# Kernel optimization log

Measured on AMD Instinct MI355X. Metric: run time of the kernel, lower is better.

Reference implementation:

```python
import jax, jax.numpy as jnp
import numpy as np

K = 4
H = 256
N0 = 65536
SIZES = [(65536, 32768), (32768, 8192), (8192, 2048)]  # (m_l, num_segments_l)


def setup_inputs() -> dict:
    key = jax.random.key(0)
    ks = jax.random.split(key, 20)
    inp = {}
    inp["x"] = jax.random.normal(ks[0], (N0, H), jnp.float32)
    inp["initial_map"] = jax.random.randint(ks[1], (N0,), 0, N0)
    prev = N0
    for l, (m, g) in enumerate(SIZES):
        # -1 is the 'no child' sentinel (maps to the prepended zero row after +1)
        inp[f"order_matrix_{l}"] = jax.random.randint(ks[2 + l], (K, m), -1, prev)
        inp[f"pooling_{l}"] = jnp.repeat(jnp.arange(g), m // g)  # covers all segments
        inp[f"type_mask_{l}"] = jax.random.randint(ks[6 + l], (m,), 0, 4)  # 0 leaf, 1 P, 2 Z, 3 S
        prev = g
    scale = 1.0 / np.sqrt(H).astype(np.float32)
    inp["W_z"] = jax.random.normal(ks[10], (K, H, H), jnp.float32) * scale
    inp["W_z_int"] = jax.random.normal(ks[11], (H, H), jnp.float32) * scale
    inp["W_s"] = jax.random.normal(ks[12], (K, H, H), jnp.float32) * scale
    inp["W_s_int"] = jax.random.normal(ks[13], (H, H), jnp.float32) * scale
    inp["W_p"] = jax.random.normal(ks[14], (H, H), jnp.float32) * scale
    inp["W_pf"] = jax.random.normal(ks[15], (H, H), jnp.float32) * scale
    return inp


def _layer(data, om, pool, tmask, g, W_z, W_z_int, W_s, W_s_int, W_p, W_pf):
    omp = om + 1                      # [K, m]; -1 -> 0 (zero row)
    empty = omp == 0                  # children that don't exist
    padded = jnp.concatenate([jnp.zeros((1, data.shape[1]), data.dtype), data], axis=0)
    gathered = padded[omp]            # [K, m, H]

    def type_sum(W):                  # per-child Linear, mask missing children, sum over children
        stack = jnp.einsum('kmh,koh->kmo', gathered, W)
        return jnp.where(empty[:, :, None], 0.0, stack).sum(axis=0)

    z_out = type_sum(W_z) @ W_z_int.T         # [m, H]
    s_out = type_sum(W_s) @ W_s_int.T         # [m, H]
    p_out = gathered[0] @ W_p.T               # [m, H]

    temp = gathered[0]                        # default: pass through first child (leaf type 0)
    temp = jnp.where((tmask == 2)[:, None], z_out, temp)
    temp = jnp.where((tmask == 3)[:, None], s_out, temp)
    temp = jnp.where((tmask == 1)[:, None], p_out, temp)
    temp = jnp.where(empty.all(axis=0)[:, None], 0.0, temp)

    pooled = jax.ops.segment_sum(temp, pool, num_segments=g)       # global_add_pool
    tm2 = jax.ops.segment_max(tmask, pool, num_segments=g)         # global_max_pool
    pooled = jnp.where((tm2 != 0)[:, None], jax.nn.elu(pooled), pooled)
    pooled = jnp.where((tm2 == 1)[:, None], pooled @ W_pf.T, pooled)
    return pooled


def reference(x, initial_map,
              order_matrix_0, pooling_0, type_mask_0,
              order_matrix_1, pooling_1, type_mask_1,
              order_matrix_2, pooling_2, type_mask_2,
              W_z, W_z_int, W_s, W_s_int, W_p, W_pf):
    oms = [order_matrix_0, order_matrix_1, order_matrix_2]
    pools = [pooling_0, pooling_1, pooling_2]
    tmasks = [type_mask_0, type_mask_1, type_mask_2]
    data = x[initial_map]
    for l, (m, g) in enumerate(SIZES):
        data = _layer(data, oms[l], pools[l], tmasks[l], g,
                      W_z, W_z_int, W_s, W_s_int, W_p, W_pf)
    return data
```

## Files before the change

### kernel.cpp

```cpp
#include <hip/hip_runtime.h>
#include <math.h>

#define H 256

typedef __attribute__((ext_vector_type(8))) short bf16x8;
typedef __attribute__((ext_vector_type(4))) float f32x4;
typedef __attribute__((ext_vector_type(4))) short short4v;

__device__ __forceinline__ short f2bf(float f) {
  union { float f; unsigned u; } x;
  x.f = f;
  unsigned r = x.u + 0x7fffu + ((x.u >> 16) & 1u);
  return (short)(r >> 16);
}
__device__ __forceinline__ float bf2f(short s) {
  union { float f; unsigned u; } x;
  x.u = ((unsigned)(unsigned short)s) << 16;
  return x.f;
}

__global__ __launch_bounds__(256) void gather_cvt_kernel(const float4* __restrict__ x,
                                                         const int* __restrict__ map,
                                                         short4v* __restrict__ out, int n) {
  int total = n * (H / 4);
  for (int idx = blockIdx.x * blockDim.x + threadIdx.x; idx < total;
       idx += gridDim.x * blockDim.x) {
    int e = idx >> 6;
    int q = idx & 63;
    float4 v = x[(size_t)map[e] * 64 + q];
    short4v s;
    s[0] = f2bf(v.x); s[1] = f2bf(v.y); s[2] = f2bf(v.z); s[3] = f2bf(v.w);
    out[idx] = s;
  }
}

__global__ __launch_bounds__(256) void wprep_kernel(
    const float* __restrict__ Wz, const float* __restrict__ Wzint,
    const float* __restrict__ Ws, const float* __restrict__ Wsint,
    const float* __restrict__ Wp, const float* __restrict__ Wpf,
    short* __restrict__ Wbf, int* __restrict__ zero_base) {
  int bid = blockIdx.x;
  int tid = threadIdx.x;
  if (bid < 2048) {
    const float* Wint = (bid < 1024) ? Wzint : Wsint;
    const float* W1 = (bid < 1024) ? Wz : Ws;
    short* out = Wbf + ((bid < 1024) ? 131072 : 393216);
    int b = bid & 1023;
    int k = b >> 8, o = b & 255;
    const float* A = Wint + (size_t)o * 256;
    const float* B = W1 + (size_t)k * 65536;
    float acc = 0.f;
#pragma unroll 8
    for (int j = 0; j < 256; ++j) acc = fmaf(A[j], B[(size_t)j * 256 + tid], acc);
    out[((size_t)k * 256 + o) * 256 + tid] = f2bf(acc);
  } else if (bid < 2176) {
    int i4 = (bid - 2048) * 256 + tid;
    int e = i4 * 4;
    const float* src = (e < 65536) ? Wp : Wpf;
    int off = (e < 65536) ? e : e - 65536;
    float4 v = *(const float4*)(src + off);
    short4v o;
    o[0] = f2bf(v.x); o[1] = f2bf(v.y); o[2] = f2bf(v.z); o[3] = f2bf(v.w);
    *(short4v*)(Wbf + e) = o;
  } else {
    if (tid < 192) zero_base[tid] = 0;
  }
}

__device__ __forceinline__ void bucket_body(const int* __restrict__ tmask, int base,
                                            int m, int g, int r,
                                            int* __restrict__ lists,
                                            int* __restrict__ counts,
                                            int* __restrict__ tm2,
                                            int* __restrict__ listF,
                                            int* __restrict__ cntF) {
  __shared__ int lc[4];
  __shared__ int lbase[4];
  int tid = threadIdx.x;
  if (tid < 4) lc[tid] = 0;
  __syncthreads();
  int i = base * 256 + tid;
  int t = 0, rank = 0;
  bool ok = i < m;
  if (ok) {
    t = tmask[i];
    rank = atomicAdd(&lc[t], 1);
  }
  __syncthreads();
  if (tid < 4) lbase[tid] = atomicAdd(&counts[tid], lc[tid]);
  __syncthreads();
  if (ok) lists[t * m + lbase[t] + rank] = i;

  int s = i;
  if (s < g) {
    int t2 = 0;
    for (int j = 0; j < r; ++j) {
      int tt = tmask[s * r + j];
      t2 = tt > t2 ? tt : t2;
    }
    tm2[s] = t2;
    unsigned long long mask = __ballot(t2 == 1);
    if (t2 == 1) {
      int lane = tid & 63;
      unsigned long long lt = (lane == 0) ? 0ull : (~0ull >> (64 - lane));
      int rnk = __popcll(mask & lt);
      int leader = __ffsll((long long)mask) - 1;
      int b = 0;
      if (lane == leader) b = atomicAdd(cntF, __popcll(mask));
      b = __shfl(b, leader);
      listF[b + rnk] = s;
    }
  }
}

__global__ __launch_bounds__(256) void bucket_all_kernel(
    const int* __restrict__ tm0, const int* __restrict__ tm1, const int* __restrict__ tm2in,
    int* __restrict__ lists0, int* __restrict__ lists1, int* __restrict__ lists2,
    int* __restrict__ counts,
    int* __restrict__ seg0, int* __restrict__ seg1, int* __restrict__ seg2,
    int* __restrict__ listF0, int* __restrict__ listF1, int* __restrict__ listF2) {
  int bid = blockIdx.x;
  if (bid < 256)
    bucket_body(tm0, bid, 65536, 32768, 2, lists0, counts, seg0, listF0, counts + 4);
  else if (bid < 384)
    bucket_body(tm1, bid - 256, 32768, 8192, 4, lists1, counts + 8, seg1, listF1, counts + 12);
  else
    bucket_body(tm2in, bid - 384, 8192, 2048, 4, lists2, counts + 16, seg2, listF2, counts + 20);
}

template <int NCH>
__device__ __forceinline__ void gemm_tile(const short* __restrict__ Abf,
                                          const int* __restrict__ om, int m,
                                          const int* __restrict__ list, int n,
                                          int rowbase, int cg,
                                          const short* __restrict__ W1,
                                          const short* __restrict__ zrow,
                                          short* __restrict__ temp, char* lds) {
  const int tid = threadIdx.x;
  const int lane = tid & 63;
  const int wave = tid >> 6;
  const int lr = lane & 15;
  const int kg = lane >> 4;
  const int wrow = rowbase + wave * 32;

  int cidx[2][NCH];
#pragma unroll
  for (int rt = 0; rt < 2; ++rt) {
    int i = wrow + rt * 16 + lr;
    int rid = (i < n) ? list[i] : -1;
#pragma unroll
    for (int k = 0; k < NCH; ++k) cidx[rt][k] = (rid >= 0) ? om[k * m + rid] : -1;
  }

  f32x4 acc[2][4];
#pragma unroll
  for (int rt = 0; rt < 2; ++rt)
#pragma unroll
    for (int c = 0; c < 4; ++c) {
      f32x4 z = {0.f, 0.f, 0.f, 0.f};
      acc[rt][c] = z;
    }

  for (int kc = 0; kc < NCH; ++kc) {
    const short* ap[2];
#pragma unroll
    for (int rt = 0; rt < 2; ++rt) {
      int c = cidx[rt][kc];
      ap[rt] = (c >= 0) ? (Abf + (size_t)c * 256 + kg * 8) : (zrow + kg * 8);
    }

    const char* psrc = (const char*)W1 + ((size_t)kc * 256 + cg * 64) * 512;
    __syncthreads();
#pragma unroll
    for (int it = 0; it < 8; ++it) {
      int idx = it * 4096 + tid * 16;
      bf16x8 v = *(const bf16x8*)(psrc + idx);
      int col = idx >> 9;
      *(bf16x8*)(lds + (idx ^ ((col & 7) << 4))) = v;
    }
    __syncthreads();

#pragma unroll
    for (int ko = 0; ko < 8; ++ko) {
      bf16x8 a[2], b[4];
#pragma unroll
      for (int c = 0; c < 4; ++c) {
        int col = c * 16 + lr;
        int off = (col * 512 + ko * 64 + kg * 16) ^ ((col & 7) << 4);
        b[c] = *(const bf16x8*)(lds + off);
      }
#pragma unroll
      for (int rt = 0; rt < 2; ++rt) a[rt] = *(const bf16x8*)(ap[rt] + ko * 32);
#pragma unroll
      for (int rt = 0; rt < 2; ++rt)
#pragma unroll
        for (int c = 0; c < 4; ++c)
          acc[rt][c] =
              __builtin_amdgcn_mfma_f32_16x16x32_bf16(a[rt], b[c], acc[rt][c], 0, 0, 0);
    }
  }

#pragma unroll
  for (int rt = 0; rt < 2; ++rt) {
#pragma unroll
    for (int q = 0; q < 4; ++q) {
      int i2 = wrow + rt * 16 + kg * 4 + q;
      if (i2 >= n) continue;
      int row = list[i2];
      short* dst = temp + (size_t)row * 256 + cg * 64 + lr;
#pragma unroll
      for (int c = 0; c < 4; ++c) dst[c * 16] = f2bf(acc[rt][c][q]);
    }
  }
}

__global__ __launch_bounds__(256) void fused_gemm(
    const short* __restrict__ Abf, const int* __restrict__ om, int m,
    const int* __restrict__ lists, const int* __restrict__ counts,
    const short* __restrict__ Wp,
    const short* __restrict__ Wcz, const short* __restrict__ Wcs,
    const short* __restrict__ zrow,
    short* __restrict__ temp) {
  const int c14 = (m >> 7) << 2;
  int bid = (int)blockIdx.x;
  __shared__ __align__(16) char lds[64 * 512];

  int type, item;
  if (bid < c14)            { type = 2; item = bid; }
  else if (bid < 2 * c14)   { type = 3; item = bid - c14; }
  else if (bid < 3 * c14)   { type = 1; item = bid - 2 * c14; }
  else                      { type = 0; item = bid - 3 * c14; }

  int n = counts[type];
  const int* list = lists + type * m;

  if (type == 0) {
    int rowbase = item * 64;
    if (rowbase >= n) return;
    int lim = n - rowbase;
    if (lim > 64) lim = 64;
    for (int idx = threadIdx.x; idx < lim * 32; idx += 256) {
      int e = rowbase + (idx >> 5);
      int q = idx & 31;
      int row = list[e];
      int c = om[row];
      bf16x8 v = {0, 0, 0, 0, 0, 0, 0, 0};
      if (c >= 0) v = *(const bf16x8*)(Abf + (size_t)c * 256 + q * 8);
      *(bf16x8*)(temp + (size_t)row * 256 + q * 8) = v;
    }
    return;
  }

  int rowbase = (item >> 2) * 128;
  int cg = item & 3;
  if (rowbase >= n) return;

  if (type == 1)
    gemm_tile<1>(Abf, om, m, list, n, rowbase, cg, Wp, zrow, temp, lds);
  else if (type == 2)
    gemm_tile<4>(Abf, om, m, list, n, rowbase, cg, Wcz, zrow, temp, lds);
  else
    gemm_tile<4>(Abf, om, m, list, n, rowbase, cg, Wcs, zrow, temp, lds);
}

__global__ __launch_bounds__(256) void reduce_kernel(const short* __restrict__ temp,
                                                     int r, int g,
                                                     const int* __restrict__ tm2,
                                                     float* __restrict__ outf,
                                                     short* __restrict__ outbf) {
  int idx = blockIdx.x * 256 + threadIdx.x;
  if (idx >= g * 32) return;
  int s = idx >> 5;
  int q = idx & 31;
  float acc[8];
#pragma unroll
  for (int k = 0; k < 8; ++k) acc[k] = 0.f;
  for (int j = 0; j < r; ++j) {
    bf16x8 v = *(const bf16x8*)(temp + (size_t)(s * r + j) * 256 + q * 8);
#pragma unroll
    for (int k = 0; k < 8; ++k) acc[k] += bf2f(v[k]);
  }
  if (tm2[s] != 0) {
#pragma unroll
    for (int k = 0; k < 8; ++k) acc[k] = acc[k] > 0.f ? acc[k] : (expf(acc[k]) - 1.f);
  }
  if (outf) {
    float4 f0 = {acc[0], acc[1], acc[2], acc[3]};
    float4 f1 = {acc[4], acc[5], acc[6], acc[7]};
    *(float4*)(outf + (size_t)s * 256 + q * 8) = f0;
    *(float4*)(outf + (size_t)s * 256 + q * 8 + 4) = f1;
  }
  if (outbf) {
    bf16x8 o;
#pragma unroll
    for (int k = 0; k < 8; ++k) o[k] = f2bf(acc[k]);
    *(bf16x8*)(outbf + (size_t)s * 256 + q * 8) = o;
  }
}

template <int SRC>
__global__ __launch_bounds__(256) void pf_gemm(short* __restrict__ buf,
                                               float* __restrict__ fbuf,
                                               const int* __restrict__ listF,
                                               const int* __restrict__ cnt,
                                               const short* __restrict__ Wpf) {
  int n = *cnt;
  int rowbase = blockIdx.x * 32;
  if (rowbase >= n) return;
  const int lane = threadIdx.x & 63;
  const int wave = threadIdx.x >> 6;
  const int colbase = wave * 64;
  const int lr = lane & 15;
  const int kg = lane >> 4;

  int src[2];
#pragma unroll
  for (int rt = 0; rt < 2; ++rt) {
    int i = rowbase + rt * 16 + lr;
    src[rt] = (i < n) ? listF[i] : -1;
  }

  f32x4 acc[2][4];
#pragma unroll
  for (int rt = 0; rt < 2; ++rt)
#pragma unroll
    for (int c = 0; c < 4; ++c) {
      f32x4 z = {0.f, 0.f, 0.f, 0.f};
      acc[rt][c] = z;
    }

#pragma unroll 2
  for (int ko = 0; ko < 256; ko += 32) {
    bf16x8 b[4];
#pragma unroll
    for (int c = 0; c < 4; ++c)
      b[c] = *(const bf16x8*)(Wpf + (size_t)(colbase + c * 16 + lr) * 256 + ko + kg * 8);
#pragma unroll
    for (int rt = 0; rt < 2; ++rt) {
      bf16x8 a = {0, 0, 0, 0, 0, 0, 0, 0};
      if (src[rt] >= 0) {
        if (SRC == 0) {
          a = *(const bf16x8*)(buf + (size_t)src[rt] * 256 + ko + kg * 8);
        } else {
          const float* p = fbuf + (size_t)src[rt] * 256 + ko + kg * 8;
          float4 u0 = *(const float4*)p;
          float4 u1 = *(const float4*)(p + 4);
          a[0] = f2bf(u0.x); a[1] = f2bf(u0.y); a[2] = f2bf(u0.z); a[3] = f2bf(u0.w);
          a[4] = f2bf(u1.x); a[5] = f2bf(u1.y); a[6] = f2bf(u1.z); a[7] = f2bf(u1.w);
        }
      }
#pragma unroll
      for (int c = 0; c < 4; ++c)
        acc[rt][c] = __builtin_amdgcn_mfma_f32_16x16x32_bf16(a, b[c], acc[rt][c], 0, 0, 0);
    }
  }

  __syncthreads();

#pragma unroll
  for (int rt = 0; rt < 2; ++rt) {
#pragma unroll
    for (int q = 0; q < 4; ++q) {
      int i2 = rowbase + rt * 16 + kg * 4 + q;
      if (i2 >= n) continue;
      int c2 = listF[i2];
      if (SRC == 0) {
        short* db = buf + (size_t)c2 * 256 + colbase + lr;
#pragma unroll
        for (int c = 0; c < 4; ++c) db[c * 16] = f2bf(acc[rt][c][q]);
      } else {
        float* df = fbuf + (size_t)c2 * 256 + colbase + lr;
#pragma unroll
        for (int c = 0; c < 4; ++c) df[c * 16] = acc[rt][c][q];
      }
    }
  }
}

extern "C" void kernel_launch(void* const* d_in, const int* in_sizes, int n_in,
                              void* d_out, int out_size, void* d_ws, size_t ws_size,
                              hipStream_t stream) {
  const float* x = (const float*)d_in[0];
  const int* initial_map = (const int*)d_in[1];
  const int* om[3] = {(const int*)d_in[2], (const int*)d_in[5], (const int*)d_in[8]};
  const int* tmask[3] = {(const int*)d_in[4], (const int*)d_in[7], (const int*)d_in[10]};
  const float* W_z = (const float*)d_in[11];
  const float* W_z_int = (const float*)d_in[12];
  const float* W_s = (const float*)d_in[13];
  const float* W_s_int = (const float*)d_in[14];
  const float* W_p = (const float*)d_in[15];
  const float* W_pf = (const float*)d_in[16];

  char* base = (char*)d_ws;
  short* d0bf  = (short*)(base);
  short* temp0 = (short*)(base + 33554432);
  short* d1bf  = (short*)(base);
  short* temp1 = (short*)(base + 16777216);
  short* d2bf  = (short*)(base + 33554432);
  short* temp2 = (short*)(base + 37748736);
  size_t off = 67108864;
  short* Wbf = (short*)(base + off); off += 655360 * 2;
  int* lists0 = (int*)(base + off); off += 4u * 65536 * 4;
  int* lists1 = (int*)(base + off); off += 4u * 32768 * 4;
  int* lists2 = (int*)(base + off); off += 4u * 8192 * 4;
  int* listF0 = (int*)(base + off); off += 32768 * 4;
  int* listF1 = (int*)(base + off); off += 8192 * 4;
  int* listF2 = (int*)(base + off); off += 2048 * 4;
  int* seg0 = (int*)(base + off); off += 32768 * 4;
  int* seg1 = (int*)(base + off); off += 8192 * 4;
  int* seg2 = (int*)(base + off); off += 2048 * 4;
  int* counts = (int*)(base + off); off += 256;
  short* zrow = (short*)(base + off); off += 512;

  short* Wp_bf  = Wbf + 0;
  short* Wpf_bf = Wbf + 65536;
  short* Wcz_bf = Wbf + 131072;
  short* Wcs_bf = Wbf + 393216;

  hipLaunchKernelGGL(wprep_kernel, dim3(2177), dim3(256), 0, stream, W_z, W_z_int,
                     W_s, W_s_int, W_p, W_pf, Wbf, counts);
  hipLaunchKernelGGL(bucket_all_kernel, dim3(416), dim3(256), 0, stream,
                     tmask[0], tmask[1], tmask[2], lists0, lists1, lists2, counts,
                     seg0, seg1, seg2, listF0, listF1, listF2);
  hipLaunchKernelGGL(gather_cvt_kernel, dim3(2048), dim3(256), 0, stream,
                     (const float4*)x, initial_map, (short4v*)d0bf, 65536);

  const int Ms[3] = {65536, 32768, 8192};
  const int Gs[3] = {32768, 8192, 2048};
  const short* dinbf[3] = {d0bf, d1bf, d2bf};
  short* tempL[3] = {temp0, temp1, temp2};
  short* nextbf[3] = {d1bf, d2bf, nullptr};
  int* listsL[3] = {lists0, lists1, lists2};
  int* listFL[3] = {listF0, listF1, listF2};
  int* segL[3] = {seg0, seg1, seg2};

  for (int l = 0; l < 3; ++l) {
    int m = Ms[l], g = Gs[l], r = m / g;
    int c14 = (m >> 7) << 2;
    int grid = 3 * c14 + m / 64;
    hipLaunchKernelGGL(fused_gemm, dim3(grid), dim3(256), 0, stream, dinbf[l], om[l],
                       m, listsL[l], counts + l * 8, Wp_bf, Wcz_bf, Wcs_bf, zrow,
                       tempL[l]);

    hipLaunchKernelGGL(reduce_kernel, dim3(g * 32 / 256), dim3(256), 0, stream,
                       tempL[l], r, g, segL[l], (l == 2) ? (float*)d_out : nullptr,
                       nextbf[l]);

    if (l < 2)
      hipLaunchKernelGGL((pf_gemm<0>), dim3(g / 32), dim3(256), 0, stream, nextbf[l],
                         (float*)nullptr, listFL[l], counts + l * 8 + 4, Wpf_bf);
    else
      hipLaunchKernelGGL((pf_gemm<1>), dim3(g / 32), dim3(256), 0, stream,
                         (short*)nullptr, (float*)d_out, listFL[l], counts + l * 8 + 4,
                         Wpf_bf);
  }
}
```

Baseline: 229.0 us.

## Compute all 256 output columns per block to reuse gathered A rows

Each GEMM block now covers the full 256-wide output (four 64-column groups) instead of a single column group, so a block handles 128 rows at full width. The gathered child rows are loaded into registers once per child rather than being re-gathered by four separate blocks. The cost is a 4x larger accumulator array (128 floats per thread) plus 64 A registers, which raises register pressure and lowers occupancy. The grid also shrinks by 4x, leaving fewer blocks to spread across the CUs.

```diff
diff --git a/kernel.cpp b/kernel.cpp
--- a/kernel.cpp
+++ b/kernel.cpp
@@ -132,7 +132,7 @@
 __device__ __forceinline__ void gemm_tile(const short* __restrict__ Abf,
                                           const int* __restrict__ om, int m,
                                           const int* __restrict__ list, int n,
-                                          int rowbase, int cg,
+                                          int rowbase,
                                           const short* __restrict__ W1,
                                           const short* __restrict__ zrow,
                                           short* __restrict__ temp, char* lds) {
@@ -152,51 +152,54 @@
     for (int k = 0; k < NCH; ++k) cidx[rt][k] = (rid >= 0) ? om[k * m + rid] : -1;
   }
 
-  f32x4 acc[2][4];
+  f32x4 acc[2][16];
 #pragma unroll
   for (int rt = 0; rt < 2; ++rt)
 #pragma unroll
-    for (int c = 0; c < 4; ++c) {
+    for (int c = 0; c < 16; ++c) {
       f32x4 z = {0.f, 0.f, 0.f, 0.f};
       acc[rt][c] = z;
     }
 
   for (int kc = 0; kc < NCH; ++kc) {
-    const short* ap[2];
+    bf16x8 areg[2][8];
 #pragma unroll
     for (int rt = 0; rt < 2; ++rt) {
       int c = cidx[rt][kc];
-      ap[rt] = (c >= 0) ? (Abf + (size_t)c * 256 + kg * 8) : (zrow + kg * 8);
-    }
-
-    const char* psrc = (const char*)W1 + ((size_t)kc * 256 + cg * 64) * 512;
-    __syncthreads();
-#pragma unroll
-    for (int it = 0; it < 8; ++it) {
-      int idx = it * 4096 + tid * 16;
-      bf16x8 v = *(const bf16x8*)(psrc + idx);
-      int col = idx >> 9;
-      *(bf16x8*)(lds + (idx ^ ((col & 7) << 4))) = v;
-    }
-    __syncthreads();
-
-#pragma unroll
-    for (int ko = 0; ko < 8; ++ko) {
-      bf16x8 a[2], b[4];
-#pragma unroll
-      for (int c = 0; c < 4; ++c) {
-        int col = c * 16 + lr;
-        int off = (col * 512 + ko * 64 + kg * 16) ^ ((col & 7) << 4);
-        b[c] = *(const bf16x8*)(lds + off);
+      const short* ap = (c >= 0) ? (Abf + (size_t)c * 256 + kg * 8) : (zrow + kg * 8);
+#pragma unroll
+      for (int ko = 0; ko < 8; ++ko) areg[rt][ko] = *(const bf16x8*)(ap + ko * 32);
+    }
+
+#pragma unroll
+    for (int cg = 0; cg < 4; ++cg) {
+      const char* psrc = (const char*)W1 + ((size_t)kc * 256 + cg * 64) * 512;
+      __syncthreads();
+#pragma unroll
+      for (int it = 0; it < 8; ++it) {
+        int idx = it * 4096 + tid * 16;
+        bf16x8 v = *(const bf16x8*)(psrc + idx);
+        int col = idx >> 9;
+        *(bf16x8*)(lds + (idx ^ ((col & 7) << 4))) = v;
       }
-#pragma unroll
-      for (int rt = 0; rt < 2; ++rt) a[rt] = *(const bf16x8*)(ap[rt] + ko * 32);
-#pragma unroll
-      for (int rt = 0; rt < 2; ++rt)
-#pragma unroll
-        for (int c = 0; c < 4; ++c)
-          acc[rt][c] =
-              __builtin_amdgcn_mfma_f32_16x16x32_bf16(a[rt], b[c], acc[rt][c], 0, 0, 0);
+      __syncthreads();
+
+#pragma unroll
+      for (int ko = 0; ko < 8; ++ko) {
+        bf16x8 b[4];
+#pragma unroll
+        for (int c = 0; c < 4; ++c) {
+          int col = c * 16 + lr;
+          int off = (col * 512 + ko * 64 + kg * 16) ^ ((col & 7) << 4);
+          b[c] = *(const bf16x8*)(lds + off);
+        }
+#pragma unroll
+        for (int rt = 0; rt < 2; ++rt)
+#pragma unroll
+          for (int c = 0; c < 4; ++c)
+            acc[rt][cg * 4 + c] = __builtin_amdgcn_mfma_f32_16x16x32_bf16(
+                areg[rt][ko], b[c], acc[rt][cg * 4 + c], 0, 0, 0);
+      }
     }
   }
 
@@ -207,9 +210,12 @@
       int i2 = wrow + rt * 16 + kg * 4 + q;
       if (i2 >= n) continue;
       int row = list[i2];
-      short* dst = temp + (size_t)row * 256 + cg * 64 + lr;
-#pragma unroll
-      for (int c = 0; c < 4; ++c) dst[c * 16] = f2bf(acc[rt][c][q]);
+      short* dst = temp + (size_t)row * 256 + lr;
+#pragma unroll
+      for (int cg = 0; cg < 4; ++cg)
+#pragma unroll
+        for (int c = 0; c < 4; ++c)
+          dst[cg * 64 + c * 16] = f2bf(acc[rt][cg * 4 + c][q]);
     }
   }
 }
@@ -221,15 +227,15 @@
     const short* __restrict__ Wcz, const short* __restrict__ Wcs,
     const short* __restrict__ zrow,
     short* __restrict__ temp) {
-  const int c14 = (m >> 7) << 2;
+  const int c1 = m >> 7;
   int bid = (int)blockIdx.x;
   __shared__ __align__(16) char lds[64 * 512];
 
   int type, item;
-  if (bid < c14)            { type = 2; item = bid; }
-  else if (bid < 2 * c14)   { type = 3; item = bid - c14; }
-  else if (bid < 3 * c14)   { type = 1; item = bid - 2 * c14; }
-  else                      { type = 0; item = bid - 3 * c14; }
+  if (bid < c1)           { type = 2; item = bid; }
+  else if (bid < 2 * c1)  { type = 3; item = bid - c1; }
+  else if (bid < 3 * c1)  { type = 1; item = bid - 2 * c1; }
+  else                    { type = 0; item = bid - 3 * c1; }
 
   int n = counts[type];
   const int* list = lists + type * m;
@@ -251,16 +257,15 @@
     return;
   }
 
-  int rowbase = (item >> 2) * 128;
-  int cg = item & 3;
+  int rowbase = item * 128;
   if (rowbase >= n) return;
 
   if (type == 1)
-    gemm_tile<1>(Abf, om, m, list, n, rowbase, cg, Wp, zrow, temp, lds);
+    gemm_tile<1>(Abf, om, m, list, n, rowbase, Wp, zrow, temp, lds);
   else if (type == 2)
-    gemm_tile<4>(Abf, om, m, list, n, rowbase, cg, Wcz, zrow, temp, lds);
+    gemm_tile<4>(Abf, om, m, list, n, rowbase, Wcz, zrow, temp, lds);
   else
-    gemm_tile<4>(Abf, om, m, list, n, rowbase, cg, Wcs, zrow, temp, lds);
+    gemm_tile<4>(Abf, om, m, list, n, rowbase, Wcs, zrow, temp, lds);
 }
 
 __global__ __launch_bounds__(256) void reduce_kernel(const short* __restrict__ temp,
@@ -436,8 +441,8 @@
 
   for (int l = 0; l < 3; ++l) {
     int m = Ms[l], g = Gs[l], r = m / g;
-    int c14 = (m >> 7) << 2;
-    int grid = 3 * c14 + m / 64;
+    int c1 = m >> 7;
+    int grid = 3 * c1 + m / 64;
     hipLaunchKernelGGL(fused_gemm, dim3(grid), dim3(256), 0, stream, dinbf[l], om[l],
                        m, listsL[l], counts + l * 8, Wp_bf, Wcz_bf, Wcs_bf, zrow,
                        tempL[l]);
```

Measured after the change: 241.8 us. 1.06x slower.
